# Kernel optimization log

Hardware: AMD Instinct MI355X
Metric: run time of the kernel (lower is better)

The kernel has to match this reference:

```python
import jax, jax.numpy as jnp
import numpy as np

B, S, D = 64, 1024, 1024
NUM_TAGS = 33            # real IOBES tags
N = NUM_TAGS + 1         # + BOS tag
BOS = N - 1
NEG_INF = -10000.0


def setup_inputs() -> dict:
    key = jax.random.key(0)
    k1, k2, k3, k4 = jax.random.split(key, 4)
    emissions = jax.random.normal(k1, (B, S, D), dtype=jnp.float32)
    tags = jax.random.randint(k2, (B, S), 0, NUM_TAGS)          # valid real tags only
    mask = jnp.ones((B, S), dtype=jnp.float32)
    W = jax.random.normal(k3, (D, N), dtype=jnp.float32) / np.sqrt(D)
    b = jnp.zeros((N,), dtype=jnp.float32)
    transitions = jax.random.uniform(k4, (N, N), minval=-0.1, maxval=0.1, dtype=jnp.float32)
    # nothing may transition INTO the BOS tag
    transitions = transitions.at[:, BOS].set(NEG_INF)
    return {"emissions": emissions, "tags": tags, "mask": mask,
            "W": W, "b": b, "transitions": transitions}


def _crf_nll(em, tags, mask, transitions):
    """em: (B,S,N) projected emissions. Returns scalar NLL (sum over batch)."""
    # ---- gold path score ----
    first = tags[:, 0]                                          # (B,)
    score = transitions[BOS, first] + jnp.take_along_axis(em[:, 0], first[:, None], axis=1)[:, 0]
    e_t = jnp.take_along_axis(em[:, 1:], tags[:, 1:, None], axis=2)[..., 0]   # (B,S-1)
    t_t = transitions[tags[:, :-1], tags[:, 1:]]                 # (B,S-1)
    score = score + jnp.sum((e_t + t_t) * mask[:, 1:], axis=1)   # (B,)

    # ---- log partition via forward algorithm (scan over time) ----
    alphas0 = transitions[BOS][None, :] + em[:, 0]               # (B,N)

    def step(alphas, xs):
        em_t, m_t = xs                                           # (B,N), (B,)
        # scores[b, prev, nxt] = alphas[b,prev] + T[prev,nxt] + em_t[b,nxt]
        scores = alphas[:, :, None] + transitions[None] + em_t[:, None, :]
        new = jax.scipy.special.logsumexp(scores, axis=1)        # (B,N)
        m = m_t[:, None]
        return m * new + (1.0 - m) * alphas, None

    xs = (jnp.swapaxes(em[:, 1:], 0, 1), jnp.swapaxes(mask[:, 1:], 0, 1))  # time-major
    alphas, _ = jax.lax.scan(step, alphas0, xs)
    partition = jax.scipy.special.logsumexp(alphas, axis=1)      # (B,)
    return -jnp.sum(score - partition)


def reference(emissions, tags, mask, W, b, transitions):
    proj = emissions @ W + b                                     # (B,S,N), dropout p=0 is identity
    loss = _crf_nll(proj, tags, mask, transitions)
    logits = proj[:, :, :-1]                                     # drop BOS column, as in torch forward
    return loss, logits
```

## Files before the change

### kernel.cpp

```cpp
#include <hip/hip_runtime.h>
#include <math.h>

#define SS 1024
#define DD 1024
#define NB 64
#define NT 34
#define NP 48
#define NC 32
#define BOSR 33

typedef __attribute__((ext_vector_type(8))) short bf16x8;
typedef __attribute__((ext_vector_type(4))) float f32x4;

#define WS_BOS   0
#define WS_PMAT  (WS_BOS + NB*SS)
#define WS_CC    (WS_PMAT + NB*NC*NP*NP)
#define WS_Z     (WS_CC + NB*NC)
#define WS_SC    (WS_Z + NB)
#define WS_BF16  (WS_SC + NB)
#define BW_WT    0
#define BW_ETA   (48*1024)

__device__ __forceinline__ float warp_sum64(float x) {
  #pragma unroll
  for (int off = 32; off > 0; off >>= 1) x += __shfl_down(x, off, 64);
  return x;
}
__device__ __forceinline__ float rfl(float x) {
  return __int_as_float(__builtin_amdgcn_readfirstlane(__float_as_int(x)));
}
__device__ __forceinline__ unsigned short f2bf(float f) {
  unsigned int u = __float_as_uint(f);
  unsigned int r = u + 0x7fffu + ((u >> 16) & 1u);
  return (unsigned short)(r >> 16);
}
__device__ __forceinline__ float bf2f(unsigned short h) {
  return __uint_as_float(((unsigned int)h) << 16);
}
__device__ __forceinline__ unsigned int pk_bf16(float a, float b) {
  unsigned int d;
  asm("v_cvt_pk_bf16_f32 %0, %1, %2" : "=v"(d) : "v"(a), "v"(b));
  return d;
}

__global__ __launch_bounds__(256) void prep(const float* __restrict__ W,
                                            const float* __restrict__ T,
                                            unsigned short* __restrict__ bw) {
  int idx = blockIdx.x * 256 + threadIdx.x;
  if (idx < 48 * 1024) {
    int n = idx >> 10, k = idx & 1023;
    float v = (n < NT) ? W[k * NT + n] : 0.0f;
    bw[BW_WT + idx] = f2bf(v);
  } else if (idx < 48 * 1024 + 48 * 64) {
    int j = idx - 48 * 1024;
    int m = j >> 6, k = j & 63;
    float v = (m < NT && k < NT) ? __expf(T[k * NT + m]) : 0.0f;
    bw[BW_ETA + j] = f2bf(v);
  }
}

__global__ __launch_bounds__(256) void gemm_chains(
    const float* __restrict__ em, const unsigned short* __restrict__ bw,
    const float* __restrict__ bias, const float* __restrict__ mask,
    float* __restrict__ logits, float* __restrict__ bos,
    float* __restrict__ Pmat, float* __restrict__ CC) {
  __shared__ float eeL[4][32][52];
  __shared__ unsigned short S[4][48][72];
  const int tid = threadIdx.x;
  const int lane = tid & 63, wv = tid >> 6;
  const int q = lane >> 4, l15 = lane & 15;
  const size_t row0 = (size_t)blockIdx.x * 128;
  const int b = (int)(row0 >> 10);
  const int cg = (((int)(row0 & 1023)) >> 5) + wv;
  const unsigned short* Wt = bw + BW_WT;

  const float* A0 = em + (row0 + (size_t)wv * 32 + l15) * DD + q * 8;

  f32x4 acc[2][3];
  f32x4 z4 = {0.f, 0.f, 0.f, 0.f};
  #pragma unroll
  for (int mt = 0; mt < 2; ++mt)
    #pragma unroll
    for (int nt = 0; nt < 3; ++nt) acc[mt][nt] = z4;

  f32x4 p0a = __builtin_nontemporal_load((const f32x4*)(A0));
  f32x4 p0b = __builtin_nontemporal_load((const f32x4*)(A0 + 4));
  f32x4 p1a = __builtin_nontemporal_load((const f32x4*)(A0 + 16 * DD));
  f32x4 p1b = __builtin_nontemporal_load((const f32x4*)(A0 + 16 * DD + 4));
  bf16x8 Bf[3], Bn[3];
  #pragma unroll
  for (int nt = 0; nt < 3; ++nt)
    Bf[nt] = *(const bf16x8*)(Wt + (nt * 16 + l15) * 1024 + q * 8);

  for (int c = 0; c < 32; ++c) {
    int cn = (c + 1 < 32 ? c + 1 : c) * 32;
    f32x4 n0a = __builtin_nontemporal_load((const f32x4*)(A0 + cn));
    f32x4 n0b = __builtin_nontemporal_load((const f32x4*)(A0 + cn + 4));
    f32x4 n1a = __builtin_nontemporal_load((const f32x4*)(A0 + 16 * DD + cn));
    f32x4 n1b = __builtin_nontemporal_load((const f32x4*)(A0 + 16 * DD + cn + 4));
    #pragma unroll
    for (int nt = 0; nt < 3; ++nt)
      Bn[nt] = *(const bf16x8*)(Wt + (nt * 16 + l15) * 1024 + cn + q * 8);
    union { unsigned int u[4]; bf16x8 v; } c0, c1;
    c0.u[0] = pk_bf16(p0a[0], p0a[1]); c0.u[1] = pk_bf16(p0a[2], p0a[3]);
    c0.u[2] = pk_bf16(p0b[0], p0b[1]); c0.u[3] = pk_bf16(p0b[2], p0b[3]);
    c1.u[0] = pk_bf16(p1a[0], p1a[1]); c1.u[1] = pk_bf16(p1a[2], p1a[3]);
    c1.u[2] = pk_bf16(p1b[0], p1b[1]); c1.u[3] = pk_bf16(p1b[2], p1b[3]);
    bf16x8 Af0 = c0.v, Af1 = c1.v;
    #pragma unroll
    for (int nt = 0; nt < 3; ++nt) {
      acc[0][nt] = __builtin_amdgcn_mfma_f32_16x16x32_bf16(Af0, Bf[nt], acc[0][nt], 0, 0, 0);
      acc[1][nt] = __builtin_amdgcn_mfma_f32_16x16x32_bf16(Af1, Bf[nt], acc[1][nt], 0, 0, 0);
    }
    p0a = n0a; p0b = n0b; p1a = n1a; p1b = n1b;
    #pragma unroll
    for (int nt = 0; nt < 3; ++nt) Bf[nt] = Bn[nt];
  }

  #pragma unroll
  for (int nt = 0; nt < 3; ++nt) {
    int col = nt * 16 + l15;
    float bj = (col < NT) ? bias[col] : 0.0f;
    #pragma unroll
    for (int mt = 0; mt < 2; ++mt) {
      #pragma unroll
      for (int r = 0; r < 4; ++r) {
        float v = acc[mt][nt][r] + bj;
        size_t rg = row0 + wv * 32 + mt * 16 + q * 4 + r;
        if (col < 33) logits[rg * 33 + col] = v;
        else if (col == 33) bos[rg] = v;
        eeL[wv][mt * 16 + q * 4 + r][col] = (col < NT) ? __expf(v) : 0.0f;
      }
    }
  }

  float mval = 0.0f;
  if (lane < 32) mval = mask[row0 + wv * 32 + lane];
  unsigned long long mb = __ballot(mval > 0.5f);
  if (cg == 0) mb &= ~1ull;

  {
    unsigned long long* p = (unsigned long long*)&S[wv][0][0];
    for (int i = lane; i < 864; i += 64) p[i] = 0ull;
  }
  if (lane < NT) S[wv][lane][lane] = 0x3F80;

  bf16x8 Ef[3][2];
  const unsigned short* eta = bw + BW_ETA;
  #pragma unroll
  for (int mt = 0; mt < 3; ++mt)
    #pragma unroll
    for (int kt = 0; kt < 2; ++kt)
      Ef[mt][kt] = *(const bf16x8*)(eta + (mt * 16 + l15) * 64 + kt * 32 + q * 8);

  float Clog = 0.0f;
  for (int tt = 0; tt < 32; ++tt) {
    if ((mb >> tt) & 1ull) {
      bf16x8 Bq[2][3];
      #pragma unroll
      for (int kt = 0; kt < 2; ++kt)
        #pragma unroll
        for (int nt = 0; nt < 3; ++nt)
          Bq[kt][nt] = *(const bf16x8*)&S[wv][nt * 16 + l15][kt * 32 + q * 8];
      f32x4 pacc[3][3];
      #pragma unroll
      for (int mt = 0; mt < 3; ++mt)
        #pragma unroll
        for (int nt = 0; nt < 3; ++nt) {
          pacc[mt][nt] = __builtin_amdgcn_mfma_f32_16x16x32_bf16(
              Ef[mt][0], Bq[0][nt], z4, 0, 0, 0);
          pacc[mt][nt] = __builtin_amdgcn_mfma_f32_16x16x32_bf16(
              Ef[mt][1], Bq[1][nt], pacc[mt][nt], 0, 0, 0);
        }
      float r = rfl(pacc[0][0][0]);
      float rin = __builtin_amdgcn_rcpf(r);
      Clog += __logf(r);
      #pragma unroll
      for (int mt = 0; mt < 3; ++mt) {
        f32x4 e4 = *(const f32x4*)&eeL[wv][tt][mt * 16 + q * 4];
        e4 = e4 * rin;
        #pragma unroll
        for (int nt = 0; nt < 3; ++nt) {
          f32x4 v = pacc[mt][nt] * e4;
          uint2 pk;
          pk.x = pk_bf16(v[0], v[1]);
          pk.y = pk_bf16(v[2], v[3]);
          *(uint2*)&S[wv][nt * 16 + l15][mt * 16 + q * 4] = pk;
        }
      }
    }
  }

  float* Pb = Pmat + (size_t)(b * NC + cg) * (NP * NP);
  #pragma unroll
  for (int i = 0; i < 9; ++i) {
    int flat = i * 64 + lane;
    int n = flat / 12, qq = flat - n * 12;
    unsigned long long pk = *(unsigned long long*)&S[wv][n][qq * 4];
    float4 o;
    o.x = bf2f((unsigned short)(pk));
    o.y = bf2f((unsigned short)(pk >> 16));
    o.z = bf2f((unsigned short)(pk >> 32));
    o.w = bf2f((unsigned short)(pk >> 48));
    *(float4*)&Pb[n * 48 + qq * 4] = o;
  }
  if (lane == 0) CC[b * NC + cg] = Clog;
}

__global__ __launch_bounds__(128) void reduceZ(
    const float* __restrict__ logits, const float* __restrict__ bos,
    const float* __restrict__ T, const float* __restrict__ Pmat,
    const float* __restrict__ CC, const int* __restrict__ tags,
    const float* __restrict__ mask, float* __restrict__ Zarr,
    float* __restrict__ scorearr) {
  const int b = blockIdx.x;
  const int tid = threadIdx.x;
  const int lane = tid & 63;

  if (tid >= 64) {
    float local = 0.0f;
    for (int t = lane; t < SS; t += 64) {
      if (t == 0) {
        int tg = tags[b * SS];
        local += T[BOSR * NT + tg] + logits[(size_t)(b * SS) * 33 + tg];
      } else {
        int tg = tags[b * SS + t];
        int tp = tags[b * SS + t - 1];
        float m = mask[b * SS + t];
        local += m * (logits[(size_t)(b * SS + t) * 33 + tg] + T[tp * NT + tg]);
      }
    }
    float w = warp_sum64(local);
    if (lane == 0) scorearr[b] = w;
    return;
  }

  __shared__ __align__(16) float shv[64];
  float a0;
  if (lane < 33)       a0 = logits[(size_t)b * SS * 33 + lane] + T[BOSR * NT + lane];
  else if (lane == 33) a0 = bos[(size_t)b * SS] + T[BOSR * NT + 33];
  else                 a0 = -INFINITY;
  float K = rfl(a0);
  float v = (lane < 48) ? __expf(a0 - K) : 0.0f;
  float C = K;
  float CCl = (lane < 32) ? CC[b * NC + lane] : 0.0f;
  const float* Pbase = Pmat + (size_t)b * NC * (NP * NP) + lane * 48;

  f32x4 Pp[12];
  if (lane < 48) {
    #pragma unroll
    for (int i = 0; i < 12; ++i) Pp[i] = *(const f32x4*)(Pbase + i * 4);
  }
  for (int c = 0; c < NC; ++c) {
    shv[lane] = v;
    f32x4 cur[12];
    #pragma unroll
    for (int i = 0; i < 12; ++i) cur[i] = Pp[i];
    if (c + 1 < NC && lane < 48) {
      #pragma unroll
      for (int i = 0; i < 12; ++i)
        Pp[i] = *(const f32x4*)(Pbase + (size_t)(c + 1) * (NP * NP) + i * 4);
    }
    float u = 0.0f;
    if (lane < 48) {
      float uu0 = 0.f, uu1 = 0.f, uu2 = 0.f, uu3 = 0.f;
      #pragma unroll
      for (int qq = 0; qq < 12; qq += 4) {
        f32x4 v0 = *(const f32x4*)&shv[qq * 4];
        f32x4 v1 = *(const f32x4*)&shv[qq * 4 + 4];
        f32x4 v2 = *(const f32x4*)&shv[qq * 4 + 8];
        f32x4 v3 = *(const f32x4*)&shv[qq * 4 + 12];
        uu0 = fmaf(cur[qq][0], v0[0], uu0);   uu0 = fmaf(cur[qq][1], v0[1], uu0);
        uu0 = fmaf(cur[qq][2], v0[2], uu0);   uu0 = fmaf(cur[qq][3], v0[3], uu0);
        uu1 = fmaf(cur[qq+1][0], v1[0], uu1); uu1 = fmaf(cur[qq+1][1], v1[1], uu1);
        uu1 = fmaf(cur[qq+1][2], v1[2], uu1); uu1 = fmaf(cur[qq+1][3], v1[3], uu1);
        uu2 = fmaf(cur[qq+2][0], v2[0], uu2); uu2 = fmaf(cur[qq+2][1], v2[1], uu2);
        uu2 = fmaf(cur[qq+2][2], v2[2], uu2); uu2 = fmaf(cur[qq+2][3], v2[3], uu2);
        uu3 = fmaf(cur[qq+3][0], v3[0], uu3); uu3 = fmaf(cur[qq+3][1], v3[1], uu3);
        uu3 = fmaf(cur[qq+3][2], v3[2], uu3); uu3 = fmaf(cur[qq+3][3], v3[3], uu3);
      }
      u = (uu0 + uu1) + (uu2 + uu3);
    }
    float r = rfl(u);
    v = u * __builtin_amdgcn_rcpf(r);
    C += __logf(r) + __shfl(CCl, c, 64);
  }
  float s = warp_sum64(v);
  if (lane == 0) Zarr[b] = C + __logf(s);
}

__global__ void finalk(const float* __restrict__ Zarr,
                       const float* __restrict__ sc, float* __restrict__ out) {
  float x = Zarr[threadIdx.x] - sc[threadIdx.x];
  float s = warp_sum64(x);
  if (threadIdx.x == 0) out[0] = s;
}

extern "C" void kernel_launch(void* const* d_in, const int* in_sizes, int n_in,
                              void* d_out, int out_size, void* d_ws, size_t ws_size,
                              hipStream_t stream) {
  const float* em   = (const float*)d_in[0];
  const int*   tags = (const int*)d_in[1];
  const float* mask = (const float*)d_in[2];
  const float* W    = (const float*)d_in[3];
  const float* bias = (const float*)d_in[4];
  const float* T    = (const float*)d_in[5];

  float* out = (float*)d_out;
  float* ws  = (float*)d_ws;
  float* bos   = ws + WS_BOS;
  float* Pmat  = ws + WS_PMAT;
  float* CC    = ws + WS_CC;
  float* Zarr  = ws + WS_Z;
  float* score = ws + WS_SC;
  unsigned short* bw = (unsigned short*)(ws + WS_BF16);
  float* logits = out + 1;

  hipLaunchKernelGGL(prep, dim3(204), dim3(256), 0, stream, W, T, bw);
  hipLaunchKernelGGL(gemm_chains, dim3(NB * SS / 128), dim3(256), 0, stream,
                     em, bw, bias, mask, logits, bos, Pmat, CC);
  hipLaunchKernelGGL(reduceZ, dim3(NB), dim3(128), 0, stream,
                     logits, bos, T, Pmat, CC, tags, mask, Zarr, score);
  hipLaunchKernelGGL(finalk, dim3(1), dim3(64), 0, stream, Zarr, score, out);
}
```

Baseline: 423.1 us.

## Stage emission tiles through LDS with coalesced loads and fuse final reduction

The GEMM A-operand is now loaded cooperatively as contiguous 16-byte chunks by the whole block, converted to bf16 and written into a double-buffered LDS tile. Each wave then reads its MFMA fragments from LDS instead of doing strided per-lane global loads. The LDS buffer is unioned with the chain-stage scratch to keep the footprint down. Separately, the final loss reduction kernel is replaced by a last-block-done atomic counter inside reduceZ, which removes one launch but adds a per-iteration barrier and an extra atomic.

```diff
diff --git a/kernel.cpp b/kernel.cpp
--- a/kernel.cpp
+++ b/kernel.cpp
@@ -17,7 +17,8 @@
 #define WS_CC    (WS_PMAT + NB*NC*NP*NP)
 #define WS_Z     (WS_CC + NB*NC)
 #define WS_SC    (WS_Z + NB)
-#define WS_BF16  (WS_SC + NB)
+#define WS_CNT   (WS_SC + NB)
+#define WS_BF16  (WS_CNT + 1)
 #define BW_WT    0
 #define BW_ETA   (48*1024)
 
@@ -42,11 +43,18 @@
   asm("v_cvt_pk_bf16_f32 %0, %1, %2" : "=v"(d) : "v"(a), "v"(b));
   return d;
 }
+__device__ __forceinline__ void lds_barrier() {
+  asm volatile("s_waitcnt lgkmcnt(0)" ::: "memory");
+  __builtin_amdgcn_s_barrier();
+  __builtin_amdgcn_sched_barrier(0);
+}
 
 __global__ __launch_bounds__(256) void prep(const float* __restrict__ W,
                                             const float* __restrict__ T,
-                                            unsigned short* __restrict__ bw) {
+                                            unsigned short* __restrict__ bw,
+                                            int* __restrict__ cnt) {
   int idx = blockIdx.x * 256 + threadIdx.x;
+  if (idx == 0) *cnt = 0;
   if (idx < 48 * 1024) {
     int n = idx >> 10, k = idx & 1023;
     float v = (n < NT) ? W[k * NT + n] : 0.0f;
@@ -64,8 +72,14 @@
     const float* __restrict__ bias, const float* __restrict__ mask,
     float* __restrict__ logits, float* __restrict__ bos,
     float* __restrict__ Pmat, float* __restrict__ CC) {
-  __shared__ float eeL[4][32][52];
-  __shared__ unsigned short S[4][48][72];
+  union SMem {
+    unsigned short At[2][128][40];
+    struct {
+      unsigned short S[4][48][72];
+      float eeL[4][32][52];
+    } ch;
+  };
+  __shared__ __align__(16) SMem sm;
   const int tid = threadIdx.x;
   const int lane = tid & 63, wv = tid >> 6;
   const int q = lane >> 4, l15 = lane & 15;
@@ -73,8 +87,7 @@
   const int b = (int)(row0 >> 10);
   const int cg = (((int)(row0 & 1023)) >> 5) + wv;
   const unsigned short* Wt = bw + BW_WT;
-
-  const float* A0 = em + (row0 + (size_t)wv * 32 + l15) * DD + q * 8;
+  const f32x4* g4 = (const f32x4*)(em + row0 * DD);
 
   f32x4 acc[2][3];
   f32x4 z4 = {0.f, 0.f, 0.f, 0.f};
@@ -83,39 +96,50 @@
     #pragma unroll
     for (int nt = 0; nt < 3; ++nt) acc[mt][nt] = z4;
 
-  f32x4 p0a = __builtin_nontemporal_load((const f32x4*)(A0));
-  f32x4 p0b = __builtin_nontemporal_load((const f32x4*)(A0 + 4));
-  f32x4 p1a = __builtin_nontemporal_load((const f32x4*)(A0 + 16 * DD));
-  f32x4 p1b = __builtin_nontemporal_load((const f32x4*)(A0 + 16 * DD + 4));
+  int sr[4], sq[4];
+  #pragma unroll
+  for (int i = 0; i < 4; ++i) { int s = tid + i * 256; sr[i] = s >> 3; sq[i] = s & 7; }
+
+  f32x4 pf[4];
+  #pragma unroll
+  for (int i = 0; i < 4; ++i)
+    pf[i] = __builtin_nontemporal_load(g4 + sr[i] * 256 + sq[i]);
   bf16x8 Bf[3], Bn[3];
   #pragma unroll
   for (int nt = 0; nt < 3; ++nt)
     Bf[nt] = *(const bf16x8*)(Wt + (nt * 16 + l15) * 1024 + q * 8);
 
   for (int c = 0; c < 32; ++c) {
-    int cn = (c + 1 < 32 ? c + 1 : c) * 32;
-    f32x4 n0a = __builtin_nontemporal_load((const f32x4*)(A0 + cn));
-    f32x4 n0b = __builtin_nontemporal_load((const f32x4*)(A0 + cn + 4));
-    f32x4 n1a = __builtin_nontemporal_load((const f32x4*)(A0 + 16 * DD + cn));
-    f32x4 n1b = __builtin_nontemporal_load((const f32x4*)(A0 + 16 * DD + cn + 4));
+    #pragma unroll
+    for (int i = 0; i < 4; ++i) {
+      uint2 pk;
+      pk.x = pk_bf16(pf[i][0], pf[i][1]);
+      pk.y = pk_bf16(pf[i][2], pf[i][3]);
+      *(uint2*)&sm.At[c & 1][sr[i]][sq[i] * 4] = pk;
+    }
+    int cn = (c + 1 < 32) ? c + 1 : c;
+    #pragma unroll
+    for (int i = 0; i < 4; ++i)
+      pf[i] = __builtin_nontemporal_load(g4 + sr[i] * 256 + cn * 8 + sq[i]);
     #pragma unroll
     for (int nt = 0; nt < 3; ++nt)
-      Bn[nt] = *(const bf16x8*)(Wt + (nt * 16 + l15) * 1024 + cn + q * 8);
-    union { unsigned int u[4]; bf16x8 v; } c0, c1;
-    c0.u[0] = pk_bf16(p0a[0], p0a[1]); c0.u[1] = pk_bf16(p0a[2], p0a[3]);
-    c0.u[2] = pk_bf16(p0b[0], p0b[1]); c0.u[3] = pk_bf16(p0b[2], p0b[3]);
-    c1.u[0] = pk_bf16(p1a[0], p1a[1]); c1.u[1] = pk_bf16(p1a[2], p1a[3]);
-    c1.u[2] = pk_bf16(p1b[0], p1b[1]); c1.u[3] = pk_bf16(p1b[2], p1b[3]);
-    bf16x8 Af0 = c0.v, Af1 = c1.v;
-    #pragma unroll
-    for (int nt = 0; nt < 3; ++nt) {
-      acc[0][nt] = __builtin_amdgcn_mfma_f32_16x16x32_bf16(Af0, Bf[nt], acc[0][nt], 0, 0, 0);
-      acc[1][nt] = __builtin_amdgcn_mfma_f32_16x16x32_bf16(Af1, Bf[nt], acc[1][nt], 0, 0, 0);
-    }
-    p0a = n0a; p0b = n0b; p1a = n1a; p1b = n1b;
+      Bn[nt] = *(const bf16x8*)(Wt + (nt * 16 + l15) * 1024 + cn * 32 + q * 8);
+    lds_barrier();
+    bf16x8 Af[2];
+    #pragma unroll
+    for (int mt = 0; mt < 2; ++mt)
+      Af[mt] = *(const bf16x8*)&sm.At[c & 1][wv * 32 + mt * 16 + l15][q * 8];
+    #pragma unroll
+    for (int mt = 0; mt < 2; ++mt)
+      #pragma unroll
+      for (int nt = 0; nt < 3; ++nt)
+        acc[mt][nt] = __builtin_amdgcn_mfma_f32_16x16x32_bf16(
+            Af[mt], Bf[nt], acc[mt][nt], 0, 0, 0);
     #pragma unroll
     for (int nt = 0; nt < 3; ++nt) Bf[nt] = Bn[nt];
   }
+
+  __syncthreads();
 
   #pragma unroll
   for (int nt = 0; nt < 3; ++nt) {
@@ -129,7 +153,7 @@
         size_t rg = row0 + wv * 32 + mt * 16 + q * 4 + r;
         if (col < 33) logits[rg * 33 + col] = v;
         else if (col == 33) bos[rg] = v;
-        eeL[wv][mt * 16 + q * 4 + r][col] = (col < NT) ? __expf(v) : 0.0f;
+        sm.ch.eeL[wv][mt * 16 + q * 4 + r][col] = (col < NT) ? __expf(v) : 0.0f;
       }
     }
   }
@@ -140,10 +164,10 @@
   if (cg == 0) mb &= ~1ull;
 
   {
-    unsigned long long* p = (unsigned long long*)&S[wv][0][0];
+    unsigned long long* p = (unsigned long long*)&sm.ch.S[wv][0][0];
     for (int i = lane; i < 864; i += 64) p[i] = 0ull;
   }
-  if (lane < NT) S[wv][lane][lane] = 0x3F80;
+  if (lane < NT) sm.ch.S[wv][lane][lane] = 0x3F80;
 
   bf16x8 Ef[3][2];
   const unsigned short* eta = bw + BW_ETA;
@@ -161,7 +185,7 @@
       for (int kt = 0; kt < 2; ++kt)
         #pragma unroll
         for (int nt = 0; nt < 3; ++nt)
-          Bq[kt][nt] = *(const bf16x8*)&S[wv][nt * 16 + l15][kt * 32 + q * 8];
+          Bq[kt][nt] = *(const bf16x8*)&sm.ch.S[wv][nt * 16 + l15][kt * 32 + q * 8];
       f32x4 pacc[3][3];
       #pragma unroll
       for (int mt = 0; mt < 3; ++mt)
@@ -177,7 +201,7 @@
       Clog += __logf(r);
       #pragma unroll
       for (int mt = 0; mt < 3; ++mt) {
-        f32x4 e4 = *(const f32x4*)&eeL[wv][tt][mt * 16 + q * 4];
+        f32x4 e4 = *(const f32x4*)&sm.ch.eeL[wv][tt][mt * 16 + q * 4];
         e4 = e4 * rin;
         #pragma unroll
         for (int nt = 0; nt < 3; ++nt) {
@@ -185,7 +209,7 @@
           uint2 pk;
           pk.x = pk_bf16(v[0], v[1]);
           pk.y = pk_bf16(v[2], v[3]);
-          *(uint2*)&S[wv][nt * 16 + l15][mt * 16 + q * 4] = pk;
+          *(uint2*)&sm.ch.S[wv][nt * 16 + l15][mt * 16 + q * 4] = pk;
         }
       }
     }
@@ -196,7 +220,7 @@
   for (int i = 0; i < 9; ++i) {
     int flat = i * 64 + lane;
     int n = flat / 12, qq = flat - n * 12;
-    unsigned long long pk = *(unsigned long long*)&S[wv][n][qq * 4];
+    unsigned long long pk = *(unsigned long long*)&sm.ch.S[wv][n][qq * 4];
     float4 o;
     o.x = bf2f((unsigned short)(pk));
     o.y = bf2f((unsigned short)(pk >> 16));
@@ -212,10 +236,13 @@
     const float* __restrict__ T, const float* __restrict__ Pmat,
     const float* __restrict__ CC, const int* __restrict__ tags,
     const float* __restrict__ mask, float* __restrict__ Zarr,
-    float* __restrict__ scorearr) {
+    float* __restrict__ scorearr, int* __restrict__ cnt,
+    float* __restrict__ out) {
   const int b = blockIdx.x;
   const int tid = threadIdx.x;
   const int lane = tid & 63;
+  __shared__ __align__(16) float shv[64];
+  __shared__ int lastflag;
 
   if (tid >= 64) {
     float local = 0.0f;
@@ -232,68 +259,72 @@
     }
     float w = warp_sum64(local);
     if (lane == 0) scorearr[b] = w;
-    return;
-  }
-
-  __shared__ __align__(16) float shv[64];
-  float a0;
-  if (lane < 33)       a0 = logits[(size_t)b * SS * 33 + lane] + T[BOSR * NT + lane];
-  else if (lane == 33) a0 = bos[(size_t)b * SS] + T[BOSR * NT + 33];
-  else                 a0 = -INFINITY;
-  float K = rfl(a0);
-  float v = (lane < 48) ? __expf(a0 - K) : 0.0f;
-  float C = K;
-  float CCl = (lane < 32) ? CC[b * NC + lane] : 0.0f;
-  const float* Pbase = Pmat + (size_t)b * NC * (NP * NP) + lane * 48;
-
-  f32x4 Pp[12];
-  if (lane < 48) {
-    #pragma unroll
-    for (int i = 0; i < 12; ++i) Pp[i] = *(const f32x4*)(Pbase + i * 4);
-  }
-  for (int c = 0; c < NC; ++c) {
-    shv[lane] = v;
-    f32x4 cur[12];
-    #pragma unroll
-    for (int i = 0; i < 12; ++i) cur[i] = Pp[i];
-    if (c + 1 < NC && lane < 48) {
-      #pragma unroll
-      for (int i = 0; i < 12; ++i)
-        Pp[i] = *(const f32x4*)(Pbase + (size_t)(c + 1) * (NP * NP) + i * 4);
-    }
-    float u = 0.0f;
+  } else {
+    float a0;
+    if (lane < 33)       a0 = logits[(size_t)b * SS * 33 + lane] + T[BOSR * NT + lane];
+    else if (lane == 33) a0 = bos[(size_t)b * SS] + T[BOSR * NT + 33];
+    else                 a0 = -INFINITY;
+    float K = rfl(a0);
+    float v = (lane < 48) ? __expf(a0 - K) : 0.0f;
+    float C = K;
+    float CCl = (lane < 32) ? CC[b * NC + lane] : 0.0f;
+    const float* Pbase = Pmat + (size_t)b * NC * (NP * NP) + lane * 48;
+
+    f32x4 Pp[12];
     if (lane < 48) {
-      float uu0 = 0.f, uu1 = 0.f, uu2 = 0.f, uu3 = 0.f;
-      #pragma unroll
-      for (int qq = 0; qq < 12; qq += 4) {
-        f32x4 v0 = *(const f32x4*)&shv[qq * 4];
-        f32x4 v1 = *(const f32x4*)&shv[qq * 4 + 4];
-        f32x4 v2 = *(const f32x4*)&shv[qq * 4 + 8];
-        f32x4 v3 = *(const f32x4*)&shv[qq * 4 + 12];
-        uu0 = fmaf(cur[qq][0], v0[0], uu0);   uu0 = fmaf(cur[qq][1], v0[1], uu0);
-        uu0 = fmaf(cur[qq][2], v0[2], uu0);   uu0 = fmaf(cur[qq][3], v0[3], uu0);
-        uu1 = fmaf(cur[qq+1][0], v1[0], uu1); uu1 = fmaf(cur[qq+1][1], v1[1], uu1);
-        uu1 = fmaf(cur[qq+1][2], v1[2], uu1); uu1 = fmaf(cur[qq+1][3], v1[3], uu1);
-        uu2 = fmaf(cur[qq+2][0], v2[0], uu2); uu2 = fmaf(cur[qq+2][1], v2[1], uu2);
-        uu2 = fmaf(cur[qq+2][2], v2[2], uu2); uu2 = fmaf(cur[qq+2][3], v2[3], uu2);
-        uu3 = fmaf(cur[qq+3][0], v3[0], uu3); uu3 = fmaf(cur[qq+3][1], v3[1], uu3);
-        uu3 = fmaf(cur[qq+3][2], v3[2], uu3); uu3 = fmaf(cur[qq+3][3], v3[3], uu3);
-      }
-      u = (uu0 + uu1) + (uu2 + uu3);
-    }
-    float r = rfl(u);
-    v = u * __builtin_amdgcn_rcpf(r);
-    C += __logf(r) + __shfl(CCl, c, 64);
-  }
-  float s = warp_sum64(v);
-  if (lane == 0) Zarr[b] = C + __logf(s);
-}
-
-__global__ void finalk(const float* __restrict__ Zarr,
-                       const float* __restrict__ sc, float* __restrict__ out) {
-  float x = Zarr[threadIdx.x] - sc[threadIdx.x];
-  float s = warp_sum64(x);
-  if (threadIdx.x == 0) out[0] = s;
+      #pragma unroll
+      for (int i = 0; i < 12; ++i) Pp[i] = *(const f32x4*)(Pbase + i * 4);
+    }
+    for (int c = 0; c < NC; ++c) {
+      shv[lane] = v;
+      f32x4 cur[12];
+      #pragma unroll
+      for (int i = 0; i < 12; ++i) cur[i] = Pp[i];
+      if (c + 1 < NC && lane < 48) {
+        #pragma unroll
+        for (int i = 0; i < 12; ++i)
+          Pp[i] = *(const f32x4*)(Pbase + (size_t)(c + 1) * (NP * NP) + i * 4);
+      }
+      float u = 0.0f;
+      if (lane < 48) {
+        float uu0 = 0.f, uu1 = 0.f, uu2 = 0.f, uu3 = 0.f;
+        #pragma unroll
+        for (int qq = 0; qq < 12; qq += 4) {
+          f32x4 v0 = *(const f32x4*)&shv[qq * 4];
+          f32x4 v1 = *(const f32x4*)&shv[qq * 4 + 4];
+          f32x4 v2 = *(const f32x4*)&shv[qq * 4 + 8];
+          f32x4 v3 = *(const f32x4*)&shv[qq * 4 + 12];
+          uu0 = fmaf(cur[qq][0], v0[0], uu0);   uu0 = fmaf(cur[qq][1], v0[1], uu0);
+          uu0 = fmaf(cur[qq][2], v0[2], uu0);   uu0 = fmaf(cur[qq][3], v0[3], uu0);
+          uu1 = fmaf(cur[qq+1][0], v1[0], uu1); uu1 = fmaf(cur[qq+1][1], v1[1], uu1);
+          uu1 = fmaf(cur[qq+1][2], v1[2], uu1); uu1 = fmaf(cur[qq+1][3], v1[3], uu1);
+          uu2 = fmaf(cur[qq+2][0], v2[0], uu2); uu2 = fmaf(cur[qq+2][1], v2[1], uu2);
+          uu2 = fmaf(cur[qq+2][2], v2[2], uu2); uu2 = fmaf(cur[qq+2][3], v2[3], uu2);
+          uu3 = fmaf(cur[qq+3][0], v3[0], uu3); uu3 = fmaf(cur[qq+3][1], v3[1], uu3);
+          uu3 = fmaf(cur[qq+3][2], v3[2], uu3); uu3 = fmaf(cur[qq+3][3], v3[3], uu3);
+        }
+        u = (uu0 + uu1) + (uu2 + uu3);
+      }
+      float r = rfl(u);
+      v = u * __builtin_amdgcn_rcpf(r);
+      C += __logf(r) + __shfl(CCl, c, 64);
+    }
+    float s = warp_sum64(v);
+    if (lane == 0) Zarr[b] = C + __logf(s);
+  }
+
+  __syncthreads();
+  if (tid == 0) {
+    __threadfence();
+    lastflag = (atomicAdd(cnt, 1) == NB - 1);
+  }
+  __syncthreads();
+  if (lastflag && tid < 64) {
+    __threadfence();
+    float x = Zarr[tid] - scorearr[tid];
+    float s2 = warp_sum64(x);
+    if (tid == 0) out[0] = s2;
+  }
 }
 
 extern "C" void kernel_launch(void* const* d_in, const int* in_sizes, int n_in,
@@ -313,13 +344,13 @@
   float* CC    = ws + WS_CC;
   float* Zarr  = ws + WS_Z;
   float* score = ws + WS_SC;
+  int*   cnt   = (int*)(ws + WS_CNT);
   unsigned short* bw = (unsigned short*)(ws + WS_BF16);
   float* logits = out + 1;
 
-  hipLaunchKernelGGL(prep, dim3(204), dim3(256), 0, stream, W, T, bw);
+  hipLaunchKernelGGL(prep, dim3(204), dim3(256), 0, stream, W, T, bw, cnt);
   hipLaunchKernelGGL(gemm_chains, dim3(NB * SS / 128), dim3(256), 0, stream,
                      em, bw, bias, mask, logits, bos, Pmat, CC);
   hipLaunchKernelGGL(reduceZ, dim3(NB), dim3(128), 0, stream,
-                     logits, bos, T, Pmat, CC, tags, mask, Zarr, score);
-  hipLaunchKernelGGL(finalk, dim3(1), dim3(64), 0, stream, Zarr, score, out);
-}
+                     logits, bos, T, Pmat, CC, tags, mask, Zarr, score, cnt, out);
+}
```

Result: no change. 415.7 us (-1.7%).
